# Optimization experiments

Measured on AMD Instinct MI355X. Metric: run time of the kernel, lower is better.

Reference implementation:

```python
import jax, jax.numpy as jnp
import numpy as np

N, E, H, NH, S, EF, K = 25000, 400000, 64, 4, 16, 8, 2
HS = H // NH  # head size


def _ln(x, w, b):
    m = x.mean(-1, keepdims=True)
    v = ((x - m) ** 2).mean(-1, keepdims=True)
    return (x - m) / jnp.sqrt(v + 1e-5) * w + b


def _seg_softmax(scores, seg, n):
    # scores: [E, NH], seg: [E] -> softmax over edges sharing the same dest node
    mx = jax.ops.segment_max(scores, seg, num_segments=n)
    e = jnp.exp(scores - mx[seg])
    s = jax.ops.segment_sum(e, seg, num_segments=n)
    return e / (s[seg] + 1e-9)


def _edge_layer(h, x_s, src, dest, ef, w1, w2, proj, gated):
    # h: [N,H] (already layer-normed). Gather, fused per-edge MLP (no bias).
    inp = jnp.concatenate([h[src], h[dest], x_s[src], x_s[dest], ef], axis=-1)  # [E,168]
    raw = jnp.maximum(inp @ w1.T, 0.0) @ w2.T  # [E,NH]
    if gated:
        w = jax.nn.sigmoid(raw)
    else:
        w = _seg_softmax(jax.nn.leaky_relu(raw) / jnp.sqrt(jnp.asarray(HS, raw.dtype)), dest, N)
    msg = h.reshape(N, NH, HS)[src] * w[:, :, None]          # [E,NH,HS]
    agg = jax.ops.segment_sum(msg, dest, num_segments=N)     # [N,NH,HS]
    return agg.reshape(N, H) @ proj.T, w


def _mlp(x, w1, b1, w2, b2):
    return jnp.maximum(x @ w1.T + b1, 0.0) @ w2.T + b2


def _forward(x, x_s, edge_features, fwd_w1, fwd_w2, fwd_proj, rev_w1, rev_w2, rev_proj,
             ln_w, ln_b, r_w1, r_b1, r_w2, r_b2, z_w1, z_b1, z_w2, z_b2,
             c_w1, c_b1, c_w2, c_b2, edge_index):
    src, dest = edge_index[0], edge_index[1]
    # forward-direction stacked attention hops
    h_fwd, fwd_ws = x, []
    for k in range(K):
        h_norm = _ln(h_fwd, ln_w, ln_b)
        msg, w = _edge_layer(h_norm, x_s, src, dest, edge_features,
                             fwd_w1[k], fwd_w2[k], fwd_proj[k], gated=False)
        h_fwd = h_fwd + msg
        fwd_ws.append(w)
    fwd_ws = jnp.stack(fwd_ws, axis=-1)  # [E,NH,K]
    # reverse-direction stacked gating hops (edge direction flipped)
    h_rev, rev_ws = x, []
    for k in range(K):
        h_norm = _ln(h_rev, ln_w, ln_b)
        msg, w = _edge_layer(h_norm, x_s, dest, src, edge_features,
                             rev_w1[k], rev_w2[k], rev_proj[k], gated=True)
        h_rev = h_rev + msg
        rev_ws.append(w)
    rev_ws = jnp.stack(rev_ws, axis=-1)  # [E,NH,K]
    messages = jnp.concatenate([h_fwd - x, h_rev - x], axis=-1)  # [N,2H]
    gate_input = jnp.concatenate([x, messages], axis=-1)          # [N,3H]
    r_gate = jax.nn.sigmoid(_mlp(gate_input, r_w1, r_b1, r_w2, r_b2))
    z_gate = jax.nn.sigmoid(_mlp(gate_input, z_w1, z_b1, z_w2, z_b2))
    cand_in = jnp.concatenate([r_gate * x, messages], axis=-1)
    cand = jnp.tanh(_mlp(cand_in, c_w1, c_b1, c_w2, c_b2))
    final_h = (1.0 - z_gate) * x + z_gate * cand
    return final_h, fwd_ws, rev_ws, z_gate, r_gate


def setup_inputs() -> dict:
    key = jax.random.key(0)
    ks = jax.random.split(key, 20)
    mlp_in = 2 * H + 2 * S + EF  # 168
    width = 2 * H                # 128
    gi, gw = 3 * H, 3 * H        # 192, 192

    def nrm(k, shape, fan_in):
        return jax.random.normal(k, shape, jnp.float32) / np.sqrt(fan_in)

    return {
        'x': jax.random.normal(ks[0], (N, H), jnp.float32),
        'x_s': jax.random.normal(ks[1], (N, S), jnp.float32),
        'edge_index': jax.random.randint(ks[2], (2, E), 0, N, jnp.int32),
        'edge_features': jax.random.normal(ks[3], (E, EF), jnp.float32),
        'fwd_w1': nrm(ks[4], (K, width, mlp_in), mlp_in),
        'fwd_w2': nrm(ks[5], (K, NH, width), width),
        'fwd_proj': nrm(ks[6], (K, H, H), H),
        'rev_w1': nrm(ks[7], (K, width, mlp_in), mlp_in),
        'rev_w2': nrm(ks[8], (K, NH, width), width),
        'rev_proj': nrm(ks[9], (K, H, H), H),
        'ln_w': jnp.ones((H,), jnp.float32),
        'ln_b': jnp.zeros((H,), jnp.float32),
        'r_w1': nrm(ks[10], (gw, gi), gi), 'r_b1': jnp.zeros((gw,), jnp.float32),
        'r_w2': nrm(ks[11], (H, gw), gw), 'r_b2': jnp.zeros((H,), jnp.float32),
        'z_w1': nrm(ks[12], (gw, gi), gi), 'z_b1': jnp.zeros((gw,), jnp.float32),
        'z_w2': nrm(ks[13], (H, gw), gw), 'z_b2': jnp.zeros((H,), jnp.float32),
        'c_w1': nrm(ks[14], (gw, gi), gi), 'c_b1': jnp.zeros((gw,), jnp.float32),
        'c_w2': nrm(ks[15], (H, gw), gw), 'c_b2': jnp.zeros((H,), jnp.float32),
    }


def reference(x, x_s, edge_index, edge_features, fwd_w1, fwd_w2, fwd_proj,
              rev_w1, rev_w2, rev_proj, ln_w, ln_b, r_w1, r_b1, r_w2, r_b2,
              z_w1, z_b1, z_w2, z_b2, c_w1, c_b1, c_w2, c_b2):
    return _forward(x, x_s, edge_features, fwd_w1, fwd_w2, fwd_proj,
                    rev_w1, rev_w2, rev_proj, ln_w, ln_b,
                    r_w1, r_b1, r_w2, r_b2, z_w1, z_b1, z_w2, z_b2,
                    c_w1, c_b1, c_w2, c_b2, edge_index)
```

## Files before the change

kernel.cpp:

```cpp
#include <hip/hip_runtime.h>
#include <math.h>

#define NN 25000
#define EE 400000
#define HH 64
#define NHEAD 4
#define SDIM 16
#define EFDIM 8
#define KHOP 2
#define MIN 168
#define WID 128
#define GIN 192
#define KP 96

typedef __attribute__((ext_vector_type(8))) short bf16x8;
typedef __attribute__((ext_vector_type(4))) float f32x4;
typedef unsigned short ushortT;
typedef unsigned int uintT;

__device__ __forceinline__ float wave_sum64(float v) {
#pragma unroll
  for (int m = 1; m <= 32; m <<= 1) v += __shfl_xor(v, m, 64);
  return v;
}

__device__ __forceinline__ ushortT f2b(float f) {
  uintT u = __float_as_uint(f);
  return (ushortT)((u + 0x7FFFu + ((u >> 16) & 1u)) >> 16);
}
__device__ __forceinline__ float b2f(ushortT h) {
  return __uint_as_float(((uintT)h) << 16);
}
__device__ __forceinline__ float b2f_lo(uintT u) { return __uint_as_float(u << 16); }
__device__ __forceinline__ float b2f_hi(uintT u) { return __uint_as_float(u & 0xffff0000u); }

__global__ void k_histo2(const int* __restrict__ src, const int* __restrict__ dst,
                         int* __restrict__ cnt_s, int* __restrict__ cnt_d) {
  int e = blockIdx.x * 256 + threadIdx.x;
  if (e < EE) {
    atomicAdd(&cnt_d[dst[e]], 1);
    atomicAdd(&cnt_s[src[e]], 1);
  }
}

__global__ void k_scan2(const int* __restrict__ cnt_d, const int* __restrict__ cnt_s,
                        int* __restrict__ rp_d, int* __restrict__ rp_s) {
  const int* cnt = blockIdx.x ? cnt_s : cnt_d;
  int* rp = blockIdx.x ? rp_s : rp_d;
  __shared__ int part[1024];
  int t = threadIdx.x;
  const int CH = (NN + 1023) / 1024;
  int base = t * CH;
  int s = 0;
  for (int i = 0; i < CH; ++i) {
    int j = base + i;
    if (j < NN) s += cnt[j];
  }
  part[t] = s;
  __syncthreads();
  for (int off = 1; off < 1024; off <<= 1) {
    int v = (t >= off) ? part[t - off] : 0;
    __syncthreads();
    part[t] += v;
    __syncthreads();
  }
  int run = (t == 0) ? 0 : part[t - 1];
  for (int i = 0; i < CH; ++i) {
    int j = base + i;
    if (j < NN) { rp[j] = run; run += cnt[j]; }
  }
  if (t == 1023) rp[NN] = run;
}

__global__ void k_scatter2(const int* __restrict__ src, const int* __restrict__ dst,
                           const int* __restrict__ rp_s, const int* __restrict__ rp_d,
                           int* __restrict__ cur_s, int* __restrict__ cur_d,
                           int* __restrict__ eid_s, int* __restrict__ eid_d) {
  int e = blockIdx.x * 256 + threadIdx.x;
  if (e < EE) {
    int nd = dst[e];
    int pd = atomicAdd(&cur_d[nd], 1);
    eid_d[rp_d[nd] + pd] = e;
    int ns = src[e];
    int ps = atomicAdd(&cur_s[ns], 1);
    eid_s[rp_s[ns] + ps] = e;
  }
}

__global__ __launch_bounds__(256) void k_sortseg2(const int* __restrict__ rp_d,
                                                  const int* __restrict__ rp_s,
                                                  int* __restrict__ eid_d,
                                                  int* __restrict__ eid_s) {
  int gw = blockIdx.x * 4 + (threadIdx.x >> 6);
  int lane = threadIdx.x & 63;
  if (gw >= 2 * NN) return;
  const int* rp = (gw < NN) ? rp_d : rp_s;
  int* eids = (gw < NN) ? eid_d : eid_s;
  int node = (gw < NN) ? gw : gw - NN;
  int beg = rp[node], end = rp[node + 1];
  int deg = end - beg;
  if (deg <= 1) return;
  if (deg <= 64) {
    int v = (lane < deg) ? eids[beg + lane] : 0x7fffffff;
#pragma unroll
    for (int k = 2; k <= 64; k <<= 1) {
#pragma unroll
      for (int j = k >> 1; j > 0; j >>= 1) {
        int other = __shfl_xor(v, j, 64);
        bool takeMin = (((lane & k) == 0) == ((lane & j) == 0));
        v = takeMin ? min(v, other) : max(v, other);
      }
    }
    if (lane < deg) eids[beg + lane] = v;
  } else if (lane == 0) {
    for (int i = beg + 1; i < end; ++i) {
      int v = eids[i];
      int j = i - 1;
      while (j >= beg && eids[j] > v) { eids[j + 1] = eids[j]; --j; }
      eids[j + 1] = v;
    }
  }
}

__global__ void k_mkpair2(const int* __restrict__ eid_d, const int* __restrict__ eid_s,
                          const int* __restrict__ src, const int* __restrict__ dst,
                          int2* __restrict__ pair_d, int2* __restrict__ pair_s) {
  int i = blockIdx.x * 256 + threadIdx.x;
  if (i < EE) {
    int e1 = eid_d[i];
    pair_d[i] = make_int2(e1, src[e1]);
    int e2 = eid_s[i];
    pair_s[i] = make_int2(e2, dst[e2]);
  }
}

__global__ void k_pack_bf(const float* __restrict__ fw1, const float* __restrict__ rw1,
                          ushortT* __restrict__ pAB_all, float* __restrict__ pE_all) {
  int y = blockIdx.y;
  const float* w1 = (y < 2) ? fw1 + (size_t)y * WID * MIN
                            : rw1 + (size_t)(y - 2) * WID * MIN;
  ushortT* pAB = pAB_all + (size_t)y * 256 * KP;
  float* pE = pE_all + (size_t)y * 8 * 128;
  int i = blockIdx.x * 256 + threadIdx.x;
  if (i < 256 * KP) {
    int j = i / KP, k = i % KP;
    float v = 0.f;
    if (k < 80) {
      int row = (j < 128) ? j : j - 128;
      int col = (j < 128) ? (k < 64 ? k : k + 64) : (k < 64 ? k + 64 : k + 80);
      v = w1[row * MIN + col];
    }
    pAB[i] = f2b(v);
  } else if (i < 256 * KP + 8 * 128) {
    int ii = i - 256 * KP;
    int f = ii >> 7, j = ii & 127;
    pE[ii] = w1[j * MIN + 160 + f];
  }
}

#define CW1 (GIN * GIN)
#define CW2 (HH * GIN)
__global__ void k_cvt6(const float* __restrict__ r_w1, const float* __restrict__ z_w1,
                       const float* __restrict__ c_w1, const float* __restrict__ r_w2,
                       const float* __restrict__ z_w2, const float* __restrict__ c_w2,
                       ushortT* __restrict__ rzw1, ushortT* __restrict__ cw1,
                       ushortT* __restrict__ rw2, ushortT* __restrict__ zw2,
                       ushortT* __restrict__ cw2) {
  int i = blockIdx.x * 256 + threadIdx.x;
  if (i < CW1) rzw1[i] = f2b(r_w1[i]);
  else if (i < 2 * CW1) rzw1[i] = f2b(z_w1[i - CW1]);
  else if (i < 3 * CW1) cw1[i - 2 * CW1] = f2b(c_w1[i - 2 * CW1]);
  else if (i < 3 * CW1 + CW2) rw2[i - 3 * CW1] = f2b(r_w2[i - 3 * CW1]);
  else if (i < 3 * CW1 + 2 * CW2) zw2[i - 3 * CW1 - CW2] = f2b(z_w2[i - 3 * CW1 - CW2]);
  else if (i < 3 * CW1 + 3 * CW2) cw2[i - 3 * CW1 - 2 * CW2] = f2b(c_w2[i - 3 * CW1 - 2 * CW2]);
}

__global__ __launch_bounds__(256) void k_ln2(const float* __restrict__ hf,
                                             const float* __restrict__ hr,
                                             const float* __restrict__ xs,
                                             const float* __restrict__ lw,
                                             const float* __restrict__ lb,
                                             ushortT* __restrict__ ncf,
                                             ushortT* __restrict__ ncr) {
  const float* h = blockIdx.y ? hr : hf;
  ushortT* nodecat = blockIdx.y ? ncr : ncf;
  int t = threadIdx.x;
  int node = blockIdx.x * 4 + (t >> 6), lane = t & 63;
  if (node >= NN) return;
  float v = h[(size_t)node * HH + lane];
  float mean = wave_sum64(v) * (1.0f / 64.0f);
  float d = v - mean;
  float var = wave_sum64(d * d) * (1.0f / 64.0f);
  nodecat[(size_t)node * KP + lane] = f2b(d * rsqrtf(var + 1e-5f) * lw[lane] + lb[lane]);
  if (lane < SDIM) {
    nodecat[(size_t)node * KP + HH + lane] = f2b(xs[(size_t)node * SDIM + lane]);
    nodecat[(size_t)node * KP + 80 + lane] = 0;
  }
}

__global__ __launch_bounds__(256) void k_proj2(
    const ushortT* __restrict__ Af, const ushortT* __restrict__ Ar,
    const ushortT* __restrict__ Wf, const ushortT* __restrict__ Wr,
    ushortT* __restrict__ Cf, ushortT* __restrict__ Cr) {
  const ushortT* A = blockIdx.y ? Ar : Af;
  const ushortT* W = blockIdx.y ? Wr : Wf;
  ushortT* C = blockIdx.y ? Cr : Cf;
  int w = threadIdx.x >> 6, l = threadIdx.x & 63;
  int m0 = blockIdx.x * 64 + w * 16;
  int rowa = m0 + (l & 15);
  int kb = l >> 4;
  bf16x8 afr0 = {0,0,0,0,0,0,0,0}, afr1 = afr0, afr2 = afr0;
  if (rowa < NN) {
    const ushortT* ap = A + (size_t)rowa * KP + kb * 8;
    afr0 = *(const bf16x8*)(ap);
    afr1 = *(const bf16x8*)(ap + 32);
    afr2 = *(const bf16x8*)(ap + 64);
  }
  int crow = m0 + (l >> 4) * 4;
  int ccol0 = l & 15;
  for (int n0 = 0; n0 < 256; n0 += 64) {
    f32x4 acc[4];
#pragma unroll
    for (int n = 0; n < 4; ++n) acc[n] = (f32x4){0.f, 0.f, 0.f, 0.f};
    const ushortT* wbase = W + (size_t)(n0 + (l & 15)) * KP + kb * 8;
#pragma unroll
    for (int n = 0; n < 4; ++n) {
      const ushortT* wp = wbase + (size_t)(16 * n) * KP;
      acc[n] = __builtin_amdgcn_mfma_f32_16x16x32_bf16(afr0, *(const bf16x8*)(wp), acc[n], 0, 0, 0);
      acc[n] = __builtin_amdgcn_mfma_f32_16x16x32_bf16(afr1, *(const bf16x8*)(wp + 32), acc[n], 0, 0, 0);
      acc[n] = __builtin_amdgcn_mfma_f32_16x16x32_bf16(afr2, *(const bf16x8*)(wp + 64), acc[n], 0, 0, 0);
    }
#pragma unroll
    for (int n = 0; n < 4; ++n) {
      int col = n0 + ccol0 + n * 16;
#pragma unroll
      for (int r = 0; r < 4; ++r) {
        int row = crow + r;
        if (row < NN) C[(size_t)row * 256 + col] = f2b(acc[n][r]);
      }
    }
  }
}

template <int ACT, int BF16OUT, int KD>
__global__ __launch_bounds__(256) void k_gemm2(
    const ushortT* __restrict__ A, int lda, const ushortT* __restrict__ W,
    const float* __restrict__ bias, void* __restrict__ Cout, int ldc, int M, int Nc) {
  constexpr int KS = KD / 32;
  int w = threadIdx.x >> 6, l = threadIdx.x & 63;
  int m0 = blockIdx.x * 64 + w * 16;
  int rowa = m0 + (l & 15);
  int kb = l >> 4;
  bf16x8 afr[KS];
#pragma unroll
  for (int ks = 0; ks < KS; ++ks) {
    afr[ks] = (bf16x8){0, 0, 0, 0, 0, 0, 0, 0};
    if (rowa < M) afr[ks] = *(const bf16x8*)(A + (size_t)rowa * lda + ks * 32 + kb * 8);
  }
  int crow = m0 + (l >> 4) * 4;
  int ccol0 = l & 15;
  for (int n0 = 0; n0 < Nc; n0 += 64) {
    f32x4 acc[4];
#pragma unroll
    for (int n = 0; n < 4; ++n) acc[n] = (f32x4){0.f, 0.f, 0.f, 0.f};
    const ushortT* wbase = W + (size_t)(n0 + (l & 15)) * KD + kb * 8;
#pragma unroll
    for (int n = 0; n < 4; ++n) {
      const ushortT* wp = wbase + (size_t)(16 * n) * KD;
#pragma unroll
      for (int ks = 0; ks < KS; ++ks)
        acc[n] = __builtin_amdgcn_mfma_f32_16x16x32_bf16(afr[ks], *(const bf16x8*)(wp + ks * 32),
                                                         acc[n], 0, 0, 0);
    }
#pragma unroll
    for (int n = 0; n < 4; ++n) {
      int col = n0 + ccol0 + n * 16;
      float bv = bias ? bias[col] : 0.f;
#pragma unroll
      for (int r = 0; r < 4; ++r) {
        int row = crow + r;
        if (row < M) {
          float v = acc[n][r] + bv;
          if (ACT == 1) v = fmaxf(v, 0.f);
          else if (ACT == 2) v = 1.f / (1.f + expf(-v));
          else if (ACT == 3) v = tanhf(v);
          if (BF16OUT)
            ((ushortT*)Cout)[(size_t)row * ldc + col] = f2b(v);
          else
            ((float*)Cout)[(size_t)row * ldc + col] = v;
        }
      }
    }
  }
}

__global__ __launch_bounds__(256) void k_edge2(
    const ushortT* __restrict__ cABf, const ushortT* __restrict__ cABr,
    const float* __restrict__ ef, const int* __restrict__ srcp,
    const int* __restrict__ dstp, const float* __restrict__ w1e_f,
    const float* __restrict__ w1e_r, const float* __restrict__ w2f,
    const float* __restrict__ w2r, float* __restrict__ rawout,
    float* __restrict__ outRW, int hop) {
  int y = blockIdx.y;
  const ushortT* cAB = y ? cABr : cABf;
  const int* idxA = y ? dstp : srcp;
  const int* idxB = y ? srcp : dstp;
  const float* w1e = y ? w1e_r : w1e_f;
  const float* w2 = y ? w2r : w2f;
  __shared__ float w1e_s[8][128];
  __shared__ float w2_s[4][128];
  int t = threadIdx.x;
  for (int i = t; i < 1024; i += 256) w1e_s[i >> 7][i & 127] = w1e[i];
  for (int i = t; i < 512; i += 256) w2_s[i >> 7][i & 127] = w2[i];
  __syncthreads();
  int es = t >> 2, q = t & 3;
  int e = blockIdx.x * 64 + es;
  int a = idxA[e], b = idxB[e];
  const ushortT* cA = cAB + (size_t)a * 256;
  const ushortT* cB = cAB + (size_t)b * 256 + 128;
  const float4* efp = (const float4*)(ef + (size_t)e * EFDIM);
  float4 e0 = efp[0], e1 = efp[1];
  float efv[8] = {e0.x, e0.y, e0.z, e0.w, e1.x, e1.y, e1.z, e1.w};
  float p[4] = {0.f, 0.f, 0.f, 0.f};
#pragma unroll
  for (int c = 0; c < 4; ++c) {
    int j = c * 32 + q * 8;
    uint4 ua4 = *(const uint4*)(cA + j);
    uint4 ub4 = *(const uint4*)(cB + j);
    const uintT* au = (const uintT*)&ua4;
    const uintT* bu = (const uintT*)&ub4;
    float h[8];
#pragma unroll
    for (int i2 = 0; i2 < 4; ++i2) {
      h[2 * i2] = b2f_lo(au[i2]) + b2f_lo(bu[i2]);
      h[2 * i2 + 1] = b2f_hi(au[i2]) + b2f_hi(bu[i2]);
    }
#pragma unroll
    for (int f = 0; f < 8; ++f) {
      float ev = efv[f];
      float4 w0 = *(const float4*)(&w1e_s[f][j]);
      float4 w1v = *(const float4*)(&w1e_s[f][j + 4]);
      h[0] += ev * w0.x; h[1] += ev * w0.y; h[2] += ev * w0.z; h[3] += ev * w0.w;
      h[4] += ev * w1v.x; h[5] += ev * w1v.y; h[6] += ev * w1v.z; h[7] += ev * w1v.w;
    }
#pragma unroll
    for (int i2 = 0; i2 < 8; ++i2) h[i2] = fmaxf(h[i2], 0.f);
#pragma unroll
    for (int o = 0; o < 4; ++o) {
      float4 u0 = *(const float4*)(&w2_s[o][j]);
      float4 u1 = *(const float4*)(&w2_s[o][j + 4]);
      p[o] += h[0] * u0.x + h[1] * u0.y + h[2] * u0.z + h[3] * u0.w +
              h[4] * u1.x + h[5] * u1.y + h[6] * u1.z + h[7] * u1.w;
    }
  }
#pragma unroll
  for (int o = 0; o < 4; ++o) {
    p[o] += __shfl_xor(p[o], 1, 64);
    p[o] += __shfl_xor(p[o], 2, 64);
  }
  float pv = (q == 0) ? p[0] : (q == 1) ? p[1] : (q == 2) ? p[2] : p[3];
  if (y) {
    outRW[(size_t)e * (NHEAD * KHOP) + q * KHOP + hop] = 1.f / (1.f + expf(-pv));
  } else {
    rawout[(size_t)e * 4 + q] = (pv > 0.f ? pv : 0.01f * pv) * 0.25f;
  }
}

template <int SM>
__global__ __launch_bounds__(256) void k_softagg(
    const ushortT* __restrict__ hn_bf, const float* __restrict__ s,
    const float* __restrict__ wsg, int hop, const int* __restrict__ rp,
    const int2* __restrict__ pair, const float* __restrict__ proj,
    float* __restrict__ h, float* __restrict__ wout) {
  __shared__ float proj_s[64][68];
  __shared__ float agg_s[4][64];
  __shared__ float w_s[4][64][4];
  int t = threadIdx.x;
  for (int i = t; i < 4096; i += 256) proj_s[i >> 6][i & 63] = proj[i];
  int wvi = t >> 6, lane = t & 63;
  int node = blockIdx.x * 4 + wvi;
  __syncthreads();

  float acc = 0.f;
  if (node < NN) {
    int beg = rp[node], end = rp[node + 1];
    int deg = end - beg;
    float mxv = 0.f, invv = 0.f;
    if (SM && deg > 0) {
      int li = lane >> 2, o = lane & 3;
      if (deg <= 64) {
        int i0 = beg + li;
        int ee4[4];
        float sv[4];
#pragma unroll
        for (int u = 0; u < 4; ++u) {
          int idx = i0 + u * 16;
          bool val = idx < end;
          int2 pr = pair[val ? idx : beg];
          ee4[u] = pr.x;
          float v = s[(size_t)pr.x * 4 + o];
          sv[u] = val ? v : -1e30f;
        }
        float mx = fmaxf(fmaxf(sv[0], sv[1]), fmaxf(sv[2], sv[3]));
#pragma unroll
        for (int m = 4; m <= 32; m <<= 1) mx = fmaxf(mx, __shfl_xor(mx, m, 64));
        float ex[4];
        float sum = 0.f;
#pragma unroll
        for (int u = 0; u < 4; ++u) {
          ex[u] = (sv[u] > -1e29f) ? expf(sv[u] - mx) : 0.f;
          sum += ex[u];
        }
#pragma unroll
        for (int m = 4; m <= 32; m <<= 1) sum += __shfl_xor(sum, m, 64);
        float inv = 1.f / (sum + 1e-9f);
#pragma unroll
        for (int u = 0; u < 4; ++u) {
          if (i0 + u * 16 < end) {
            float wv = ex[u] * inv;
            wout[(size_t)ee4[u] * (NHEAD * KHOP) + o * KHOP + hop] = wv;
            w_s[wvi][li + u * 16][o] = wv;
          }
        }
      } else {
        float mx = -1e30f;
        for (int ii = beg + li; ii < end; ii += 16)
          mx = fmaxf(mx, s[(size_t)pair[ii].x * 4 + o]);
#pragma unroll
        for (int m = 4; m <= 32; m <<= 1) mx = fmaxf(mx, __shfl_xor(mx, m, 64));
        float sum = 0.f;
        for (int ii = beg + li; ii < end; ii += 16)
          sum += expf(s[(size_t)pair[ii].x * 4 + o] - mx);
#pragma unroll
        for (int m = 4; m <= 32; m <<= 1) sum += __shfl_xor(sum, m, 64);
        float inv = 1.f / (sum + 1e-9f);
        for (int ii = beg + li; ii < end; ii += 16) {
          int e = pair[ii].x;
          wout[(size_t)e * (NHEAD * KHOP) + o * KHOP + hop] =
              expf(s[(size_t)e * 4 + o] - mx) * inv;
        }
        mxv = mx;
        invv = inv;
      }
    }
    int hd = lane >> 4;
    int hd2 = hd * KHOP + hop;
    float mx_hd = 0.f, inv_hd = 0.f;
    if (SM) {
      mx_hd = __shfl(mxv, hd, 64);
      inv_hd = __shfl(invv, hd, 64);
    }
    bool useLds = (deg <= 64);
    for (int ii = beg; ii < end; ii += 8) {
      int idxv[8];
      int2 pr[8];
      float wv8[8];
      float hv[8];
#pragma unroll
      for (int u = 0; u < 8; ++u) {
        int idx = ii + u;
        idxv[u] = (idx < end) ? idx : beg;
      }
#pragma unroll
      for (int u = 0; u < 8; ++u) pr[u] = pair[idxv[u]];
#pragma unroll
      for (int u = 0; u < 8; ++u) {
        if (SM) {
          if (useLds)
            wv8[u] = w_s[wvi][idxv[u] - beg][hd];
          else
            wv8[u] = expf(s[(size_t)pr[u].x * 4 + hd] - mx_hd) * inv_hd;
        } else {
          wv8[u] = wsg[(size_t)pr[u].x * (NHEAD * KHOP) + hd2];
        }
      }
#pragma unroll
      for (int u = 0; u < 8; ++u)
        hv[u] = b2f(hn_bf[(size_t)pr[u].y * KP + lane]);
#pragma unroll
      for (int u = 0; u < 8; ++u) {
        float w = (ii + u < end) ? wv8[u] : 0.f;
        acc += w * hv[u];
      }
    }
  }
  agg_s[wvi][lane] = acc;
  __syncthreads();
  if (node < NN) {
    float m = 0.f;
#pragma unroll
    for (int hh = 0; hh < 64; hh += 4) {
      float4 p = *(const float4*)(&proj_s[lane][hh]);
      m += p.x * agg_s[wvi][hh] + p.y * agg_s[wvi][hh + 1] +
           p.z * agg_s[wvi][hh + 2] + p.w * agg_s[wvi][hh + 3];
    }
    h[(size_t)node * HH + lane] += m;
  }
}

__global__ void k_gatein(const float* __restrict__ x, const float* __restrict__ hf,
                         const float* __restrict__ hr, ushortT* __restrict__ gi) {
  int g = blockIdx.x * 256 + threadIdx.x;
  if (g >= NN * HH) return;
  int node = g >> 6, j = g & 63;
  float xv = x[g];
  gi[(size_t)node * GIN + j] = f2b(xv);
  gi[(size_t)node * GIN + 64 + j] = f2b(hf[g] - xv);
  gi[(size_t)node * GIN + 128 + j] = f2b(hr[g] - xv);
}

__global__ void k_candin(const float* __restrict__ x, const float* __restrict__ r,
                         ushortT* __restrict__ gi) {
  int g = blockIdx.x * 256 + threadIdx.x;
  if (g >= NN * HH) return;
  gi[(size_t)(g >> 6) * GIN + (g & 63)] = f2b(r[g] * x[g]);
}

__global__ void k_final(const float* __restrict__ x, const float* __restrict__ zv,
                        const float* __restrict__ cand, float* __restrict__ outF) {
  int g = blockIdx.x * 256 + threadIdx.x;
  if (g >= NN * HH) return;
  float z = zv[g];
  outF[g] = (1.f - z) * x[g] + z * cand[g];
}

extern "C" void kernel_launch(void* const* d_in, const int* in_sizes, int n_in,
                              void* d_out, int out_size, void* d_ws, size_t ws_size,
                              hipStream_t stream) {
  const float* x = (const float*)d_in[0];
  const float* xs = (const float*)d_in[1];
  const int* ei = (const int*)d_in[2];
  const float* ef = (const float*)d_in[3];
  const float* fw1 = (const float*)d_in[4];
  const float* fw2 = (const float*)d_in[5];
  const float* fpj = (const float*)d_in[6];
  const float* rw1 = (const float*)d_in[7];
  const float* rw2 = (const float*)d_in[8];
  const float* rpj = (const float*)d_in[9];
  const float* lnw = (const float*)d_in[10];
  const float* lnb = (const float*)d_in[11];
  const float* r_w1 = (const float*)d_in[12];
  const float* r_b1 = (const float*)d_in[13];
  const float* r_w2 = (const float*)d_in[14];
  const float* r_b2 = (const float*)d_in[15];
  const float* z_w1 = (const float*)d_in[16];
  const float* z_b1 = (const float*)d_in[17];
  const float* z_w2 = (const float*)d_in[18];
  const float* z_b2 = (const float*)d_in[19];
  const float* c_w1 = (const float*)d_in[20];
  const float* c_b1 = (const float*)d_in[21];
  const float* c_w2 = (const float*)d_in[22];
  const float* c_b2 = (const float*)d_in[23];
  const int* srcp = ei;
  const int* dstp = ei + EE;

  float* outF = (float*)d_out;
  float* outFW = outF + (size_t)NN * HH;
  float* outRW = outFW + (size_t)EE * NHEAD * KHOP;
  float* outZ = outRW + (size_t)EE * NHEAD * KHOP;
  float* outR = outZ + (size_t)NN * HH;

  char* Wb = (char*)d_ws;
  size_t off = 0;
  auto alloc = [&](size_t bytes) -> void* {
    void* p = Wb + off;
    off += (bytes + 255) & ~(size_t)255;
    return p;
  };
  float* h_fwd = (float*)alloc((size_t)NN * HH * 4);
  float* h_rev = (float*)alloc((size_t)NN * HH * 4);
  ushortT* ncat_f = (ushortT*)alloc((size_t)NN * KP * 2);
  ushortT* ncat_r = (ushortT*)alloc((size_t)NN * KP * 2);
  float* raw = (float*)alloc((size_t)EE * NHEAD * 4);
  char* big = (char*)alloc((size_t)2 * NN * 256 * 2);
  ushortT* cAB_f = (ushortT*)big;
  ushortT* cAB_r = (ushortT*)(big + (size_t)NN * 256 * 2);
  ushortT* hid_bf = (ushortT*)big;
  ushortT* gi_bf = (ushortT*)alloc((size_t)NN * GIN * 2);
  float* cand = (float*)alloc((size_t)NN * HH * 4);
  ushortT* packAB_bf = (ushortT*)alloc((size_t)4 * 256 * KP * 2);
  float* packE = (float*)alloc((size_t)4 * 8 * 128 * 4);
  ushortT* rzw1_bf = (ushortT*)alloc((size_t)384 * GIN * 2);
  ushortT* rw2_bf = (ushortT*)alloc((size_t)HH * GIN * 2);
  ushortT* zw2_bf = (ushortT*)alloc((size_t)HH * GIN * 2);
  ushortT* cw1_bf = (ushortT*)alloc((size_t)GIN * GIN * 2);
  ushortT* cw2_bf = (ushortT*)alloc((size_t)HH * GIN * 2);
  float* rz_b1 = (float*)alloc(384 * 4);
  int* rp_d = (int*)alloc((NN + 8) * 4);
  int* rp_s = (int*)alloc((NN + 8) * 4);
  int* cur2 = (int*)alloc((size_t)2 * NN * 4);
  int* cur_d = cur2;
  int* cur_s = cur2 + NN;
  int* eid_d = (int*)alloc((size_t)EE * 4);
  int* eid_s = (int*)alloc((size_t)EE * 4);
  int2* pair_d = (int2*)alloc((size_t)EE * 8);
  int2* pair_s = (int2*)alloc((size_t)EE * 8);

  hipMemcpyAsync(h_fwd, x, (size_t)NN * HH * 4, hipMemcpyDeviceToDevice, stream);
  hipMemcpyAsync(h_rev, x, (size_t)NN * HH * 4, hipMemcpyDeviceToDevice, stream);
  hipMemcpyAsync(rz_b1, r_b1, GIN * 4, hipMemcpyDeviceToDevice, stream);
  hipMemcpyAsync(rz_b1 + GIN, z_b1, GIN * 4, hipMemcpyDeviceToDevice, stream);

  const int EB = (EE + 255) / 256, NW = (NN + 3) / 4;
  const int PB = (256 * KP + 8 * 128 + 255) / 256;

  dim3 gPack(PB, 4);
  k_pack_bf<<<gPack, 256, 0, stream>>>(fw1, rw1, packAB_bf, packE);
  k_cvt6<<<(3 * CW1 + 3 * CW2 + 255) / 256, 256, 0, stream>>>(
      r_w1, z_w1, c_w1, r_w2, z_w2, c_w2, rzw1_bf, cw1_bf, rw2_bf, zw2_bf, cw2_bf);

  hipMemsetAsync(cur2, 0, (size_t)2 * NN * 4, stream);
  k_histo2<<<EB, 256, 0, stream>>>(srcp, dstp, cur_s, cur_d);
  k_scan2<<<2, 1024, 0, stream>>>(cur_d, cur_s, rp_d, rp_s);
  hipMemsetAsync(cur2, 0, (size_t)2 * NN * 4, stream);
  k_scatter2<<<EB, 256, 0, stream>>>(srcp, dstp, rp_s, rp_d, cur_s, cur_d, eid_s, eid_d);
  k_sortseg2<<<(2 * NN + 3) / 4, 256, 0, stream>>>(rp_d, rp_s, eid_d, eid_s);
  k_mkpair2<<<EB, 256, 0, stream>>>(eid_d, eid_s, srcp, dstp, pair_d, pair_s);

  const int MB64 = (NN + 63) / 64;
  dim3 gLN(NW, 2), gProj(MB64, 2), gEdge(EE / 64, 2);
  for (int k = 0; k < KHOP; ++k) {
    k_ln2<<<gLN, 256, 0, stream>>>(h_fwd, h_rev, xs, lnw, lnb, ncat_f, ncat_r);
    k_proj2<<<gProj, 256, 0, stream>>>(ncat_f, ncat_r,
                                       packAB_bf + (size_t)k * 256 * KP,
                                       packAB_bf + (size_t)(2 + k) * 256 * KP,
                                       cAB_f, cAB_r);
    k_edge2<<<gEdge, 256, 0, stream>>>(cAB_f, cAB_r, ef, srcp, dstp,
                                       packE + (size_t)k * 8 * 128,
                                       packE + (size_t)(2 + k) * 8 * 128,
                                       fw2 + (size_t)k * NHEAD * WID,
                                       rw2 + (size_t)k * NHEAD * WID, raw, outRW, k);
    k_softagg<1><<<NW, 256, 0, stream>>>(ncat_f, raw, nullptr, k, rp_d, pair_d,
                                         fpj + (size_t)k * HH * HH, h_fwd, outFW);
    k_softagg<0><<<NW, 256, 0, stream>>>(ncat_r, nullptr, outRW, k, rp_s, pair_s,
                                         rpj + (size_t)k * HH * HH, h_rev, nullptr);
  }

  k_gatein<<<(NN * HH) / 256, 256, 0, stream>>>(x, h_fwd, h_rev, gi_bf);
  k_gemm2<1, 1, GIN><<<MB64, 256, 0, stream>>>(gi_bf, GIN, rzw1_bf, rz_b1, hid_bf,
                                               384, NN, 384);
  k_gemm2<2, 0, GIN><<<MB64, 256, 0, stream>>>(hid_bf, 384, rw2_bf, r_b2, outR, HH,
                                               NN, HH);
  k_gemm2<2, 0, GIN><<<MB64, 256, 0, stream>>>(hid_bf + GIN, 384, zw2_bf, z_b2, outZ,
                                               HH, NN, HH);
  k_candin<<<(NN * HH) / 256, 256, 0, stream>>>(x, outR, gi_bf);
  k_gemm2<1, 1, GIN><<<MB64, 256, 0, stream>>>(gi_bf, GIN, cw1_bf, c_b1, hid_bf, GIN,
                                               NN, GIN);
  k_gemm2<3, 0, GIN><<<MB64, 256, 0, stream>>>(hid_bf, GIN, cw2_bf, c_b2, cand, HH,
                                               NN, HH);
  k_final<<<(NN * HH) / 256, 256, 0, stream>>>(x, outZ, cand, outF);
}
```

Baseline: 611.5 us.

## Process edges in destination-sorted order and fuse final GRU blend into GEMM

Edge scoring now walks edges in CSR-sorted order using precomputed int4 position records and reordered edge-feature copies. Its per-edge scores and gates are written sequentially, so the aggregation kernels read them contiguously instead of gathering through edge ids. The r/z second-layer GEMMs merge into one two-way launch, and the final (1-z)x + z*tanh blend is fused into the candidate GEMM epilogue, removing a separate elementwise kernel and the cand buffer. In exchange the setup pass writes extra sorted copies of indices and features, and outRW still needs a scattered write.

```diff
diff --git a/kernel.cpp b/kernel.cpp
--- a/kernel.cpp
+++ b/kernel.cpp
@@ -122,18 +122,24 @@
   }
 }
 
-__global__ void k_mkpair2(const int* __restrict__ eid_d, const int* __restrict__ eid_s,
-                          const int* __restrict__ src, const int* __restrict__ dst,
-                          int2* __restrict__ pair_d, int2* __restrict__ pair_s) {
+__global__ void k_mkpos2(const int* __restrict__ eid_d, const int* __restrict__ eid_s,
+                         const int* __restrict__ src, const int* __restrict__ dst,
+                         const float* __restrict__ ef, int4* __restrict__ pos_f,
+                         int4* __restrict__ pos_r, float4* __restrict__ efs_f,
+                         float4* __restrict__ efs_r) {
   int i = blockIdx.x * 256 + threadIdx.x;
-  if (i < EE) {
-    int e1 = eid_d[i];
-    pair_d[i] = make_int2(e1, src[e1]);
-    int e2 = eid_s[i];
-    pair_s[i] = make_int2(e2, dst[e2]);
-  }
-}
-
+  if (i >= EE) return;
+  int e1 = eid_d[i];
+  pos_f[i] = make_int4(e1, src[e1], dst[e1], 0);
+  int e2 = eid_s[i];
+  pos_r[i] = make_int4(e2, dst[e2], src[e2], 0);
+  efs_f[2 * i] = *(const float4*)(ef + (size_t)e1 * EFDIM);
+  efs_f[2 * i + 1] = *(const float4*)(ef + (size_t)e1 * EFDIM + 4);
+  efs_r[2 * i] = *(const float4*)(ef + (size_t)e2 * EFDIM);
+  efs_r[2 * i + 1] = *(const float4*)(ef + (size_t)e2 * EFDIM + 4);
+}
+
+#define PACKN (256 * KP + 8 * 128)
 __global__ void k_pack_bf(const float* __restrict__ fw1, const float* __restrict__ rw1,
                           ushortT* __restrict__ pAB_all, float* __restrict__ pE_all) {
   int y = blockIdx.y;
@@ -151,7 +157,7 @@
       v = w1[row * MIN + col];
     }
     pAB[i] = f2b(v);
-  } else if (i < 256 * KP + 8 * 128) {
+  } else if (i < PACKN) {
     int ii = i - 256 * KP;
     int f = ii >> 7, j = ii & 127;
     pE[ii] = w1[j * MIN + 160 + f];
@@ -245,7 +251,8 @@
 template <int ACT, int BF16OUT, int KD>
 __global__ __launch_bounds__(256) void k_gemm2(
     const ushortT* __restrict__ A, int lda, const ushortT* __restrict__ W,
-    const float* __restrict__ bias, void* __restrict__ Cout, int ldc, int M, int Nc) {
+    const float* __restrict__ bias, void* __restrict__ Cout, int ldc, int M, int Nc,
+    const float* __restrict__ zv, const float* __restrict__ xp) {
   constexpr int KS = KD / 32;
   int w = threadIdx.x >> 6, l = threadIdx.x & 63;
   int m0 = blockIdx.x * 64 + w * 16;
@@ -284,6 +291,11 @@
           if (ACT == 1) v = fmaxf(v, 0.f);
           else if (ACT == 2) v = 1.f / (1.f + expf(-v));
           else if (ACT == 3) v = tanhf(v);
+          else if (ACT == 5) {
+            float z = zv[(size_t)row * HH + col];
+            float xv = xp[(size_t)row * HH + col];
+            v = (1.f - z) * xv + z * tanhf(v);
+          }
           if (BF16OUT)
             ((ushortT*)Cout)[(size_t)row * ldc + col] = f2b(v);
           else
@@ -294,17 +306,67 @@
   }
 }
 
-__global__ __launch_bounds__(256) void k_edge2(
+__global__ __launch_bounds__(256) void k_gemm_rz(
+    const ushortT* __restrict__ hid, const ushortT* __restrict__ rw2,
+    const ushortT* __restrict__ zw2, const float* __restrict__ rb2,
+    const float* __restrict__ zb2, float* __restrict__ outR, float* __restrict__ outZ) {
+  int y = blockIdx.y;
+  const ushortT* A = hid + (y ? GIN : 0);
+  const ushortT* W = y ? zw2 : rw2;
+  const float* bias = y ? zb2 : rb2;
+  float* C = y ? outZ : outR;
+  constexpr int KS = GIN / 32;
+  int w = threadIdx.x >> 6, l = threadIdx.x & 63;
+  int m0 = blockIdx.x * 64 + w * 16;
+  int rowa = m0 + (l & 15);
+  int kb = l >> 4;
+  bf16x8 afr[KS];
+#pragma unroll
+  for (int ks = 0; ks < KS; ++ks) {
+    afr[ks] = (bf16x8){0, 0, 0, 0, 0, 0, 0, 0};
+    if (rowa < NN) afr[ks] = *(const bf16x8*)(A + (size_t)rowa * 384 + ks * 32 + kb * 8);
+  }
+  int crow = m0 + (l >> 4) * 4;
+  int ccol0 = l & 15;
+  f32x4 acc[4];
+#pragma unroll
+  for (int n = 0; n < 4; ++n) acc[n] = (f32x4){0.f, 0.f, 0.f, 0.f};
+  const ushortT* wbase = W + (size_t)(l & 15) * GIN + kb * 8;
+#pragma unroll
+  for (int n = 0; n < 4; ++n) {
+    const ushortT* wp = wbase + (size_t)(16 * n) * GIN;
+#pragma unroll
+    for (int ks = 0; ks < KS; ++ks)
+      acc[n] = __builtin_amdgcn_mfma_f32_16x16x32_bf16(afr[ks], *(const bf16x8*)(wp + ks * 32),
+                                                       acc[n], 0, 0, 0);
+  }
+#pragma unroll
+  for (int n = 0; n < 4; ++n) {
+    int col = ccol0 + n * 16;
+    float bv = bias[col];
+#pragma unroll
+    for (int r = 0; r < 4; ++r) {
+      int row = crow + r;
+      if (row < NN) {
+        float v = acc[n][r] + bv;
+        C[(size_t)row * HH + col] = 1.f / (1.f + expf(-v));
+      }
+    }
+  }
+}
+
+__global__ __launch_bounds__(256) void k_edge3(
     const ushortT* __restrict__ cABf, const ushortT* __restrict__ cABr,
-    const float* __restrict__ ef, const int* __restrict__ srcp,
-    const int* __restrict__ dstp, const float* __restrict__ w1e_f,
-    const float* __restrict__ w1e_r, const float* __restrict__ w2f,
-    const float* __restrict__ w2r, float* __restrict__ rawout,
-    float* __restrict__ outRW, int hop) {
+    const int4* __restrict__ pos_f, const int4* __restrict__ pos_r,
+    const float4* __restrict__ efs_f, const float4* __restrict__ efs_r,
+    const float* __restrict__ w1e_f, const float* __restrict__ w1e_r,
+    const float* __restrict__ w2f, const float* __restrict__ w2r,
+    float* __restrict__ s_seq, float* __restrict__ outRW,
+    float* __restrict__ ws_seq, int hop) {
   int y = blockIdx.y;
   const ushortT* cAB = y ? cABr : cABf;
-  const int* idxA = y ? dstp : srcp;
-  const int* idxB = y ? srcp : dstp;
+  const int4* pos = y ? pos_r : pos_f;
+  const float4* efs = y ? efs_r : efs_f;
   const float* w1e = y ? w1e_r : w1e_f;
   const float* w2 = y ? w2r : w2f;
   __shared__ float w1e_s[8][128];
@@ -314,19 +376,18 @@
   for (int i = t; i < 512; i += 256) w2_s[i >> 7][i & 127] = w2[i];
   __syncthreads();
   int es = t >> 2, q = t & 3;
-  int e = blockIdx.x * 64 + es;
-  int a = idxA[e], b = idxB[e];
-  const ushortT* cA = cAB + (size_t)a * 256;
-  const ushortT* cB = cAB + (size_t)b * 256 + 128;
-  const float4* efp = (const float4*)(ef + (size_t)e * EFDIM);
-  float4 e0 = efp[0], e1 = efp[1];
+  size_t ii = (size_t)blockIdx.x * 64 + es;
+  int4 pr = pos[ii];
+  const ushortT* cA = cAB + (size_t)pr.y * 256;
+  const ushortT* cBp = cAB + (size_t)pr.z * 256 + 128;
+  float4 e0 = efs[2 * ii], e1 = efs[2 * ii + 1];
   float efv[8] = {e0.x, e0.y, e0.z, e0.w, e1.x, e1.y, e1.z, e1.w};
   float p[4] = {0.f, 0.f, 0.f, 0.f};
 #pragma unroll
   for (int c = 0; c < 4; ++c) {
     int j = c * 32 + q * 8;
     uint4 ua4 = *(const uint4*)(cA + j);
-    uint4 ub4 = *(const uint4*)(cB + j);
+    uint4 ub4 = *(const uint4*)(cBp + j);
     const uintT* au = (const uintT*)&ua4;
     const uintT* bu = (const uintT*)&ub4;
     float h[8];
@@ -360,17 +421,19 @@
   }
   float pv = (q == 0) ? p[0] : (q == 1) ? p[1] : (q == 2) ? p[2] : p[3];
   if (y) {
-    outRW[(size_t)e * (NHEAD * KHOP) + q * KHOP + hop] = 1.f / (1.f + expf(-pv));
+    float sig = 1.f / (1.f + expf(-pv));
+    outRW[(size_t)pr.x * (NHEAD * KHOP) + q * KHOP + hop] = sig;
+    ws_seq[ii * 4 + q] = sig;
   } else {
-    rawout[(size_t)e * 4 + q] = (pv > 0.f ? pv : 0.01f * pv) * 0.25f;
+    s_seq[ii * 4 + q] = (pv > 0.f ? pv : 0.01f * pv) * 0.25f;
   }
 }
 
 template <int SM>
 __global__ __launch_bounds__(256) void k_softagg(
-    const ushortT* __restrict__ hn_bf, const float* __restrict__ s,
-    const float* __restrict__ wsg, int hop, const int* __restrict__ rp,
-    const int2* __restrict__ pair, const float* __restrict__ proj,
+    const ushortT* __restrict__ hn_bf, const float* __restrict__ s_seq,
+    const float* __restrict__ ws_seq, int hop, const int* __restrict__ rp,
+    const int4* __restrict__ pos, const float* __restrict__ proj,
     float* __restrict__ h, float* __restrict__ wout) {
   __shared__ float proj_s[64][68];
   __shared__ float agg_s[4][64];
@@ -396,9 +459,9 @@
         for (int u = 0; u < 4; ++u) {
           int idx = i0 + u * 16;
           bool val = idx < end;
-          int2 pr = pair[val ? idx : beg];
-          ee4[u] = pr.x;
-          float v = s[(size_t)pr.x * 4 + o];
+          int id2 = val ? idx : beg;
+          ee4[u] = pos[id2].x;
+          float v = s_seq[(size_t)id2 * 4 + o];
           sv[u] = val ? v : -1e30f;
         }
         float mx = fmaxf(fmaxf(sv[0], sv[1]), fmaxf(sv[2], sv[3]));
@@ -425,26 +488,24 @@
       } else {
         float mx = -1e30f;
         for (int ii = beg + li; ii < end; ii += 16)
-          mx = fmaxf(mx, s[(size_t)pair[ii].x * 4 + o]);
+          mx = fmaxf(mx, s_seq[(size_t)ii * 4 + o]);
 #pragma unroll
         for (int m = 4; m <= 32; m <<= 1) mx = fmaxf(mx, __shfl_xor(mx, m, 64));
         float sum = 0.f;
         for (int ii = beg + li; ii < end; ii += 16)
-          sum += expf(s[(size_t)pair[ii].x * 4 + o] - mx);
+          sum += expf(s_seq[(size_t)ii * 4 + o] - mx);
 #pragma unroll
         for (int m = 4; m <= 32; m <<= 1) sum += __shfl_xor(sum, m, 64);
         float inv = 1.f / (sum + 1e-9f);
         for (int ii = beg + li; ii < end; ii += 16) {
-          int e = pair[ii].x;
-          wout[(size_t)e * (NHEAD * KHOP) + o * KHOP + hop] =
-              expf(s[(size_t)e * 4 + o] - mx) * inv;
+          wout[(size_t)pos[ii].x * (NHEAD * KHOP) + o * KHOP + hop] =
+              expf(s_seq[(size_t)ii * 4 + o] - mx) * inv;
         }
         mxv = mx;
         invv = inv;
       }
     }
     int hd = lane >> 4;
-    int hd2 = hd * KHOP + hop;
     float mx_hd = 0.f, inv_hd = 0.f;
     if (SM) {
       mx_hd = __shfl(mxv, hd, 64);
@@ -453,7 +514,7 @@
     bool useLds = (deg <= 64);
     for (int ii = beg; ii < end; ii += 8) {
       int idxv[8];
-      int2 pr[8];
+      int other[8];
       float wv8[8];
       float hv[8];
 #pragma unroll
@@ -462,21 +523,21 @@
         idxv[u] = (idx < end) ? idx : beg;
       }
 #pragma unroll
-      for (int u = 0; u < 8; ++u) pr[u] = pair[idxv[u]];
+      for (int u = 0; u < 8; ++u) other[u] = pos[idxv[u]].y;
 #pragma unroll
       for (int u = 0; u < 8; ++u) {
         if (SM) {
           if (useLds)
             wv8[u] = w_s[wvi][idxv[u] - beg][hd];
           else
-            wv8[u] = expf(s[(size_t)pr[u].x * 4 + hd] - mx_hd) * inv_hd;
+            wv8[u] = expf(s_seq[(size_t)idxv[u] * 4 + hd] - mx_hd) * inv_hd;
         } else {
-          wv8[u] = wsg[(size_t)pr[u].x * (NHEAD * KHOP) + hd2];
+          wv8[u] = ws_seq[(size_t)idxv[u] * 4 + hd];
         }
       }
 #pragma unroll
       for (int u = 0; u < 8; ++u)
-        hv[u] = b2f(hn_bf[(size_t)pr[u].y * KP + lane]);
+        hv[u] = b2f(hn_bf[(size_t)other[u] * KP + lane]);
 #pragma unroll
       for (int u = 0; u < 8; ++u) {
         float w = (ii + u < end) ? wv8[u] : 0.f;
@@ -514,14 +575,6 @@
   int g = blockIdx.x * 256 + threadIdx.x;
   if (g >= NN * HH) return;
   gi[(size_t)(g >> 6) * GIN + (g & 63)] = f2b(r[g] * x[g]);
-}
-
-__global__ void k_final(const float* __restrict__ x, const float* __restrict__ zv,
-                        const float* __restrict__ cand, float* __restrict__ outF) {
-  int g = blockIdx.x * 256 + threadIdx.x;
-  if (g >= NN * HH) return;
-  float z = zv[g];
-  outF[g] = (1.f - z) * x[g] + z * cand[g];
 }
 
 extern "C" void kernel_launch(void* const* d_in, const int* in_sizes, int n_in,
@@ -571,13 +624,13 @@
   float* h_rev = (float*)alloc((size_t)NN * HH * 4);
   ushortT* ncat_f = (ushortT*)alloc((size_t)NN * KP * 2);
   ushortT* ncat_r = (ushortT*)alloc((size_t)NN * KP * 2);
-  float* raw = (float*)alloc((size_t)EE * NHEAD * 4);
+  float* s_seq = (float*)alloc((size_t)EE * NHEAD * 4);
+  float* ws_seq = (float*)alloc((size_t)EE * NHEAD * 4);
   char* big = (char*)alloc((size_t)2 * NN * 256 * 2);
   ushortT* cAB_f = (ushortT*)big;
   ushortT* cAB_r = (ushortT*)(big + (size_t)NN * 256 * 2);
   ushortT* hid_bf = (ushortT*)big;
   ushortT* gi_bf = (ushortT*)alloc((size_t)NN * GIN * 2);
-  float* cand = (float*)alloc((size_t)NN * HH * 4);
   ushortT* packAB_bf = (ushortT*)alloc((size_t)4 * 256 * KP * 2);
   float* packE = (float*)alloc((size_t)4 * 8 * 128 * 4);
   ushortT* rzw1_bf = (ushortT*)alloc((size_t)384 * GIN * 2);
@@ -593,29 +646,31 @@
   int* cur_s = cur2 + NN;
   int* eid_d = (int*)alloc((size_t)EE * 4);
   int* eid_s = (int*)alloc((size_t)EE * 4);
-  int2* pair_d = (int2*)alloc((size_t)EE * 8);
-  int2* pair_s = (int2*)alloc((size_t)EE * 8);
-
-  hipMemcpyAsync(h_fwd, x, (size_t)NN * HH * 4, hipMemcpyDeviceToDevice, stream);
-  hipMemcpyAsync(h_rev, x, (size_t)NN * HH * 4, hipMemcpyDeviceToDevice, stream);
-  hipMemcpyAsync(rz_b1, r_b1, GIN * 4, hipMemcpyDeviceToDevice, stream);
-  hipMemcpyAsync(rz_b1 + GIN, z_b1, GIN * 4, hipMemcpyDeviceToDevice, stream);
+  int4* pos_f = (int4*)alloc((size_t)EE * 16);
+  int4* pos_r = (int4*)alloc((size_t)EE * 16);
+  float4* efs_f = (float4*)alloc((size_t)EE * 32);
+  float4* efs_r = (float4*)alloc((size_t)EE * 32);
+
+  (void)hipMemcpyAsync(h_fwd, x, (size_t)NN * HH * 4, hipMemcpyDeviceToDevice, stream);
+  (void)hipMemcpyAsync(h_rev, x, (size_t)NN * HH * 4, hipMemcpyDeviceToDevice, stream);
+  (void)hipMemcpyAsync(rz_b1, r_b1, GIN * 4, hipMemcpyDeviceToDevice, stream);
+  (void)hipMemcpyAsync(rz_b1 + GIN, z_b1, GIN * 4, hipMemcpyDeviceToDevice, stream);
 
   const int EB = (EE + 255) / 256, NW = (NN + 3) / 4;
-  const int PB = (256 * KP + 8 * 128 + 255) / 256;
+  const int PB = (PACKN + 255) / 256;
 
   dim3 gPack(PB, 4);
   k_pack_bf<<<gPack, 256, 0, stream>>>(fw1, rw1, packAB_bf, packE);
   k_cvt6<<<(3 * CW1 + 3 * CW2 + 255) / 256, 256, 0, stream>>>(
       r_w1, z_w1, c_w1, r_w2, z_w2, c_w2, rzw1_bf, cw1_bf, rw2_bf, zw2_bf, cw2_bf);
 
-  hipMemsetAsync(cur2, 0, (size_t)2 * NN * 4, stream);
+  (void)hipMemsetAsync(cur2, 0, (size_t)2 * NN * 4, stream);
   k_histo2<<<EB, 256, 0, stream>>>(srcp, dstp, cur_s, cur_d);
   k_scan2<<<2, 1024, 0, stream>>>(cur_d, cur_s, rp_d, rp_s);
-  hipMemsetAsync(cur2, 0, (size_t)2 * NN * 4, stream);
+  (void)hipMemsetAsync(cur2, 0, (size_t)2 * NN * 4, stream);
   k_scatter2<<<EB, 256, 0, stream>>>(srcp, dstp, rp_s, rp_d, cur_s, cur_d, eid_s, eid_d);
   k_sortseg2<<<(2 * NN + 3) / 4, 256, 0, stream>>>(rp_d, rp_s, eid_d, eid_s);
-  k_mkpair2<<<EB, 256, 0, stream>>>(eid_d, eid_s, srcp, dstp, pair_d, pair_s);
+  k_mkpos2<<<EB, 256, 0, stream>>>(eid_d, eid_s, srcp, dstp, ef, pos_f, pos_r, efs_f, efs_r);
 
   const int MB64 = (NN + 63) / 64;
   dim3 gLN(NW, 2), gProj(MB64, 2), gEdge(EE / 64, 2);
@@ -625,28 +680,26 @@
                                        packAB_bf + (size_t)k * 256 * KP,
                                        packAB_bf + (size_t)(2 + k) * 256 * KP,
                                        cAB_f, cAB_r);
-    k_edge2<<<gEdge, 256, 0, stream>>>(cAB_f, cAB_r, ef, srcp, dstp,
+    k_edge3<<<gEdge, 256, 0, stream>>>(cAB_f, cAB_r, pos_f, pos_r, efs_f, efs_r,
                                        packE + (size_t)k * 8 * 128,
                                        packE + (size_t)(2 + k) * 8 * 128,
                                        fw2 + (size_t)k * NHEAD * WID,
-                                       rw2 + (size_t)k * NHEAD * WID, raw, outRW, k);
-    k_softagg<1><<<NW, 256, 0, stream>>>(ncat_f, raw, nullptr, k, rp_d, pair_d,
+                                       rw2 + (size_t)k * NHEAD * WID,
+                                       s_seq, outRW, ws_seq, k);
+    k_softagg<1><<<NW, 256, 0, stream>>>(ncat_f, s_seq, nullptr, k, rp_d, pos_f,
                                          fpj + (size_t)k * HH * HH, h_fwd, outFW);
-    k_softagg<0><<<NW, 256, 0, stream>>>(ncat_r, nullptr, outRW, k, rp_s, pair_s,
+    k_softagg<0><<<NW, 256, 0, stream>>>(ncat_r, nullptr, ws_seq, k, rp_s, pos_r,
                                          rpj + (size_t)k * HH * HH, h_rev, nullptr);
   }
 
   k_gatein<<<(NN * HH) / 256, 256, 0, stream>>>(x, h_fwd, h_rev, gi_bf);
   k_gemm2<1, 1, GIN><<<MB64, 256, 0, stream>>>(gi_bf, GIN, rzw1_bf, rz_b1, hid_bf,
-                                               384, NN, 384);
-  k_gemm2<2, 0, GIN><<<MB64, 256, 0, stream>>>(hid_bf, 384, rw2_bf, r_b2, outR, HH,
-                                               NN, HH);
-  k_gemm2<2, 0, GIN><<<MB64, 256, 0, stream>>>(hid_bf + GIN, 384, zw2_bf, z_b2, outZ,
-                                               HH, NN, HH);
+                                               384, NN, 384, nullptr, nullptr);
+  dim3 gRZ(MB64, 2);
+  k_gemm_rz<<<gRZ, 256, 0, stream>>>(hid_bf, rw2_bf, zw2_bf, r_b2, z_b2, outR, outZ);
   k_candin<<<(NN * HH) / 256, 256, 0, stream>>>(x, outR, gi_bf);
   k_gemm2<1, 1, GIN><<<MB64, 256, 0, stream>>>(gi_bf, GIN, cw1_bf, c_b1, hid_bf, GIN,
-                                               NN, GIN);
-  k_gemm2<3, 0, GIN><<<MB64, 256, 0, stream>>>(hid_bf, GIN, cw2_bf, c_b2, cand, HH,
-                                               NN, HH);
-  k_final<<<(NN * HH) / 256, 256, 0, stream>>>(x, outZ, cand, outF);
-}
+                                               NN, GIN, nullptr, nullptr);
+  k_gemm2<5, 0, GIN><<<MB64, 256, 0, stream>>>(hid_bf, GIN, cw2_bf, c_b2, outF, HH,
+                                               NN, HH, outZ, x);
+}
```

Result: no change. 609.5 us (-0.3%).
